# Performance work log

Hardware: AMD Instinct MI355X
Metric: run time of the kernel (lower is better)

## Reference

```python
import jax, jax.numpy as jnp
import numpy as np


def _conv1d(x, w, b):
    # x: (N, C_in, L), w: (C_out, C_in, K=5), padding=2, stride=1 (torch Conv1d semantics)
    y = jax.lax.conv_general_dilated(x, w, window_strides=(1,), padding=[(2, 2)],
                                     dimension_numbers=('NCH', 'OIH', 'NCH'))
    return y + b[None, :, None]


def _conv_block(x, w, b):
    # Conv1d -> ReLU -> MaxPool1d(kernel=2, stride=2)
    y = jax.nn.relu(_conv1d(x, w, b))
    n, c, l = y.shape
    return y.reshape(n, c, l // 2, 2).max(axis=-1)


def setup_inputs() -> dict:
    key = jax.random.key(0)
    ks = jax.random.split(key, 20)

    def lin(k, shape, fan_in):
        bound = 1.0 / np.sqrt(fan_in)
        return jax.random.uniform(k, shape, jnp.float32, -bound, bound)

    inp = {
        'x': jax.random.normal(ks[0], (1, 64, 1024), jnp.float32),
        'topo_map': jax.random.uniform(ks[1], (64, 64), jnp.float32),
        # 64 stacked tiny attention nets: Linear(64->128), Linear(128->64), no bias
        'W1': lin(ks[2], (64, 128, 64), 64),
        'W2': lin(ks[3], (64, 64, 128), 128),
        'c1_w': lin(ks[4], (32, 64, 5), 64 * 5),  'c1_b': lin(ks[5], (32,), 64 * 5),
        'c2_w': lin(ks[6], (16, 32, 5), 32 * 5),  'c2_b': lin(ks[7], (16,), 32 * 5),
        'c3_w': lin(ks[8], (8, 16, 5), 16 * 5),   'c3_b': lin(ks[9], (8,), 16 * 5),
        'c4_w': lin(ks[10], (4, 8, 5), 8 * 5),    'c4_b': lin(ks[11], (4,), 8 * 5),
        'c5_w': lin(ks[12], (2, 4, 5), 4 * 5),    'c5_b': lin(ks[13], (2,), 4 * 5),
        'c6_w': lin(ks[14], (1, 2, 5), 2 * 5),    'c6_b': lin(ks[15], (1,), 2 * 5),
        'out_w': lin(ks[16], (1, 16), 16),        'out_b': lin(ks[17], (1,), 16),
    }
    return inp


def reference(x, topo_map, W1, W2, c1_w, c1_b, c2_w, c2_b, c3_w, c3_b,
              c4_w, c4_b, c5_w, c5_b, c6_w, c6_b, out_w, out_b):
    # xmean: (1, 64) -- mean over time of the single trial
    xmean = x[0].mean(axis=1)[None, :]
    att = xmean * topo_map                                  # (64, 64); row i fed to net i
    # Batched replacement for the 64 sequential tiny MLPs (no CPU round-trip):
    h = jax.nn.relu(jnp.einsum('ik,ihk->ih', att, W1))      # (64, 128)
    attn = jax.nn.sigmoid(jnp.einsum('ih,ioh->io', h, W2))  # (64, 64)
    y = attn[None] @ x                                      # (1, 64, 1024)
    for w, b in ((c1_w, c1_b), (c2_w, c2_b), (c3_w, c3_b),
                 (c4_w, c4_b), (c5_w, c5_b), (c6_w, c6_b)):
        y = _conv_block(y, w, b)                            # L halves each block: 1024 -> 16
    out = y @ out_w.T + out_b                               # (1, 1, 16) @ (16, 1) -> (1, 1, 1)
    return out.reshape(1, 1)
```

## Files before the change

kernel.cpp:

```cpp
#include <hip/hip_runtime.h>
#include <math.h>

__global__ __launch_bounds__(256) void k_xmean(const float* __restrict__ x,
                                               double* __restrict__ xmean) {
    const int c = blockIdx.x;
    const int t = threadIdx.x;
    const float* row = x + c * 1024;
    double s = 0.0;
#pragma unroll
    for (int u = 0; u < 4; ++u) s += (double)row[t + u * 256];
#pragma unroll
    for (int off = 32; off >= 1; off >>= 1) s += __shfl_down(s, off, 64);
    __shared__ double wsum[4];
    if ((t & 63) == 0) wsum[t >> 6] = s;
    __syncthreads();
    if (t == 0) xmean[c] = (wsum[0] + wsum[1] + wsum[2] + wsum[3]) * (1.0 / 1024.0);
}

__global__ __launch_bounds__(256) void k_mlp(const float* __restrict__ topo,
                                             const float* __restrict__ W1,
                                             const float* __restrict__ W2,
                                             const double* __restrict__ xmean,
                                             double* __restrict__ attn) {
    const int i = blockIdx.x;
    const int t = threadIdx.x;
    __shared__ double att[64];
    __shared__ double h[128];
    if (t < 64) att[t] = xmean[t] * (double)topo[i * 64 + t];
    __syncthreads();
    {
        const int hh = t >> 1, half = t & 1;
        const float4* wp = (const float4*)(W1 + i * 8192 + hh * 64 + half * 32);
        double acc = 0.0;
#pragma unroll
        for (int q = 0; q < 8; ++q) {
            float4 w = wp[q];
            const int k = half * 32 + q * 4;
            acc += att[k + 0] * (double)w.x + att[k + 1] * (double)w.y +
                   att[k + 2] * (double)w.z + att[k + 3] * (double)w.w;
        }
        acc += __shfl_xor(acc, 1, 64);
        if (half == 0) h[hh] = acc > 0.0 ? acc : 0.0;
    }
    __syncthreads();
    {
        const int o = t >> 2, part = t & 3;
        const float4* wp = (const float4*)(W2 + i * 8192 + o * 128 + part * 32);
        double acc = 0.0;
#pragma unroll
        for (int q = 0; q < 8; ++q) {
            float4 w = wp[q];
            const int k = part * 32 + q * 4;
            acc += h[k + 0] * (double)w.x + h[k + 1] * (double)w.y +
                   h[k + 2] * (double)w.z + h[k + 3] * (double)w.w;
        }
        acc += __shfl_xor(acc, 1, 64);
        acc += __shfl_xor(acc, 2, 64);
        if (part == 0) attn[i * 64 + o] = 1.0 / (1.0 + exp(-acc));
    }
}

__global__ __launch_bounds__(256) void k_front(const float* __restrict__ x,
                                               const double* __restrict__ attn_g,
                                               const float* __restrict__ c1w,
                                               const float* __restrict__ c1b,
                                               const float* __restrict__ c2w,
                                               const float* __restrict__ c2b,
                                               float* __restrict__ s2out) {
    const int b = blockIdx.x;
    const int t = threadIdx.x;
    const int p0 = b * 2;
    const int lbase = 8 * b - 6;
    const int rbase = 4 * b - 2;

    __shared__ float attn_l[64 * 64];
    __shared__ float x_l[64 * 20];
    __shared__ float y_l[64 * 20];
    __shared__ float w2_l[16 * 32 * 5];
    __shared__ float b1_l[32];
    __shared__ float b2_l[16];
    __shared__ float c1_l[32 * 8];
    __shared__ float c2pre[16 * 4];

    for (int e = t; e < 4096; e += 256) attn_l[e] = (float)attn_g[e];
    for (int e = t; e < 64 * 20; e += 256) {
        const int j = e / 20, li = e % 20, l = lbase + li;
        x_l[e] = (l >= 0 && l < 1024) ? x[j * 1024 + l] : 0.f;
    }
    for (int e = t; e < 2560; e += 256) w2_l[e] = c2w[e];
    if (t < 32) b1_l[t] = c1b[t];
    if (t < 16) b2_l[t] = c2b[t];
    __syncthreads();

    if (t < 128) {
        const int ig = t >> 2, lg = t & 3;
        const int i0 = ig * 2, l0 = lg * 5;
        double acc0[5] = {0, 0, 0, 0, 0}, acc1[5] = {0, 0, 0, 0, 0};
        for (int j = 0; j < 64; ++j) {
            const double a0 = (double)attn_l[i0 * 64 + j];
            const double a1 = (double)attn_l[(i0 + 1) * 64 + j];
#pragma unroll
            for (int c = 0; c < 5; ++c) {
                const double xv = (double)x_l[j * 20 + l0 + c];
                acc0[c] += a0 * xv;
                acc1[c] += a1 * xv;
            }
        }
#pragma unroll
        for (int c = 0; c < 5; ++c) {
            y_l[i0 * 20 + l0 + c]       = (float)acc0[c];
            y_l[(i0 + 1) * 20 + l0 + c] = (float)acc1[c];
        }
    }
    __syncthreads();

    {
        const int oc = t >> 3, rg = (t >> 2) & 1, icq = t & 3;
        const int sb = 8 * rg;
        double acc[8] = {0, 0, 0, 0, 0, 0, 0, 0};
        for (int ic = icq * 16; ic < icq * 16 + 16; ++ic) {
            const float* wrow = &c1w[(oc * 64 + ic) * 5];
            const float* yrow = &y_l[ic * 20 + sb];
            float yv[12];
#pragma unroll
            for (int c = 0; c < 12; ++c) yv[c] = yrow[c];
            float wv[5];
#pragma unroll
            for (int k = 0; k < 5; ++k) wv[k] = wrow[k];
#pragma unroll
            for (int k = 0; k < 5; ++k) {
                const double w = (double)wv[k];
#pragma unroll
                for (int u = 0; u < 8; ++u) acc[u] += w * (double)yv[u + k];
            }
        }
#pragma unroll
        for (int u = 0; u < 8; ++u) {
            acc[u] += __shfl_xor(acc[u], 1, 64);
            acc[u] += __shfl_xor(acc[u], 2, 64);
        }
        if (icq == 0) {
            const double bias = (double)b1_l[oc];
#pragma unroll
            for (int v = 0; v < 4; ++v) {
                const double v0 = acc[2 * v] + bias, v1 = acc[2 * v + 1] + bias;
                const double m = fmax(fmax(v0, v1), 0.0);
                const int r_idx = rg * 4 + v;
                const int r = rbase + r_idx;
                c1_l[oc * 8 + r_idx] = (r >= 0 && r < 512) ? (float)m : 0.f;
            }
        }
    }
    __syncthreads();

    if (t < 64) {
        const int oc = t >> 2, q_idx = t & 3;
        double acc = (double)b2_l[oc];
        for (int ic = 0; ic < 32; ++ic) {
            const float* wrow = &w2_l[(oc * 32 + ic) * 5];
            const float* crow = &c1_l[ic * 8 + q_idx];
#pragma unroll
            for (int k = 0; k < 5; ++k) acc += (double)wrow[k] * (double)crow[k];
        }
        c2pre[t] = (float)fmax(acc, 0.0);
    }
    __syncthreads();
    if (t < 32) {
        const int oc = t >> 1, p_idx = t & 1;
        const float m = fmaxf(c2pre[oc * 4 + 2 * p_idx], c2pre[oc * 4 + 2 * p_idx + 1]);
        s2out[oc * 256 + p0 + p_idx] = m;
    }
}

__global__ __launch_bounds__(256) void k_tail(const float* __restrict__ s2,
                                              const float* __restrict__ c3w, const float* __restrict__ c3b,
                                              const float* __restrict__ c4w, const float* __restrict__ c4b,
                                              const float* __restrict__ c5w, const float* __restrict__ c5b,
                                              const float* __restrict__ c6w, const float* __restrict__ c6b,
                                              const float* __restrict__ ow,  const float* __restrict__ ob,
                                              float* __restrict__ out) {
    const int t = threadIdx.x;
    __shared__ __align__(16) float s2p[16 * 264];
    __shared__ float w3_l[640], b3_l[8];
    __shared__ float s3_l[8 * 128];
    __shared__ float w4_l[160], b4_l[4];
    __shared__ float s4_l[4 * 64];
    __shared__ float w5_l[40],  b5_l[2];
    __shared__ float s5_l[2 * 32];
    __shared__ float w6_l[10],  b6_l[1];
    __shared__ float s6_l[16];
    __shared__ float ow_l[16],  ob_l[1];

    for (int e = t; e < 16 * 264; e += 256) s2p[e] = 0.f;
    for (int e = t; e < 640; e += 256) w3_l[e] = c3w[e];
    if (t < 8)   b3_l[t] = c3b[t];
    if (t < 160) w4_l[t] = c4w[t];
    if (t < 4)   b4_l[t] = c4b[t];
    if (t < 40)  w5_l[t] = c5w[t];
    if (t < 2)   b5_l[t] = c5b[t];
    if (t < 10)  w6_l[t] = c6w[t];
    if (t == 0)  b6_l[0] = c6b[0];
    if (t < 16)  ow_l[t] = ow[t];
    if (t == 0)  ob_l[0] = ob[0];
    __syncthreads();
    for (int e = t; e < 4096; e += 256) {
        const int ic = e >> 8, col = e & 255;
        s2p[ic * 264 + 4 + col] = s2[e];
    }
    __syncthreads();

    {
        const int oc = t >> 5, pg = t & 31;
        double acc[8] = {0, 0, 0, 0, 0, 0, 0, 0};
        for (int ic = 0; ic < 16; ++ic) {
            const float4* win4 = (const float4*)&s2p[ic * 264 + 8 * pg];
            float win[16];
#pragma unroll
            for (int q = 0; q < 4; ++q) {
                const float4 v = win4[q];
                win[4 * q] = v.x; win[4 * q + 1] = v.y; win[4 * q + 2] = v.z; win[4 * q + 3] = v.w;
            }
            const float* wrow = &w3_l[(oc * 16 + ic) * 5];
#pragma unroll
            for (int k = 0; k < 5; ++k) {
                const double w = (double)wrow[k];
#pragma unroll
                for (int u = 0; u < 8; ++u) acc[u] += w * (double)win[u + k + 2];
            }
        }
        const double bias = (double)b3_l[oc];
#pragma unroll
        for (int v = 0; v < 4; ++v) {
            const double v0 = acc[2 * v] + bias, v1 = acc[2 * v + 1] + bias;
            s3_l[oc * 128 + pg * 4 + v] = (float)fmax(fmax(v0, v1), 0.0);
        }
    }
    __syncthreads();

    {
        const int oc = t >> 6, p = t & 63;
        double a0 = (double)b4_l[oc], a1 = a0;
        for (int ic = 0; ic < 8; ++ic) {
            const float* wrow = &w4_l[(oc * 8 + ic) * 5];
            const float* srow = &s3_l[ic * 128];
            float c[6];
#pragma unroll
            for (int u = 0; u < 6; ++u) {
                const int col = 2 * p - 2 + u;
                c[u] = (col >= 0 && col < 128) ? srow[col] : 0.f;
            }
#pragma unroll
            for (int k = 0; k < 5; ++k) {
                const double w = (double)wrow[k];
                a0 += w * (double)c[k];
                a1 += w * (double)c[k + 1];
            }
        }
        s4_l[oc * 64 + p] = (float)fmax(fmax(a0, a1), 0.0);
    }
    __syncthreads();

    if (t < 64) {
        const int oc = t >> 5, p = t & 31;
        double a0 = (double)b5_l[oc], a1 = a0;
        for (int ic = 0; ic < 4; ++ic) {
            const float* wrow = &w5_l[(oc * 4 + ic) * 5];
            const float* srow = &s4_l[ic * 64];
            float c[6];
#pragma unroll
            for (int u = 0; u < 6; ++u) {
                const int col = 2 * p - 2 + u;
                c[u] = (col >= 0 && col < 64) ? srow[col] : 0.f;
            }
#pragma unroll
            for (int k = 0; k < 5; ++k) {
                const double w = (double)wrow[k];
                a0 += w * (double)c[k];
                a1 += w * (double)c[k + 1];
            }
        }
        s5_l[oc * 32 + p] = (float)fmax(fmax(a0, a1), 0.0);
    }
    __syncthreads();

    if (t < 16) {
        const int p = t;
        double a0 = (double)b6_l[0], a1 = a0;
        for (int ic = 0; ic < 2; ++ic) {
            const float* wrow = &w6_l[ic * 5];
            const float* srow = &s5_l[ic * 32];
            float c[6];
#pragma unroll
            for (int u = 0; u < 6; ++u) {
                const int col = 2 * p - 2 + u;
                c[u] = (col >= 0 && col < 32) ? srow[col] : 0.f;
            }
#pragma unroll
            for (int k = 0; k < 5; ++k) {
                const double w = (double)wrow[k];
                a0 += w * (double)c[k];
                a1 += w * (double)c[k + 1];
            }
        }
        s6_l[p] = (float)fmax(fmax(a0, a1), 0.0);
    }
    __syncthreads();

    if (t == 0) {
        double acc = (double)ob_l[0];
#pragma unroll
        for (int l = 0; l < 16; ++l) acc += (double)ow_l[l] * (double)s6_l[l];
        out[0] = (float)acc;
    }
}

extern "C" void kernel_launch(void* const* d_in, const int* in_sizes, int n_in,
                              void* d_out, int out_size, void* d_ws, size_t ws_size,
                              hipStream_t stream) {
    (void)in_sizes; (void)n_in; (void)out_size; (void)ws_size;
    const float* x    = (const float*)d_in[0];
    const float* topo = (const float*)d_in[1];
    const float* W1   = (const float*)d_in[2];
    const float* W2   = (const float*)d_in[3];
    const float* c1w  = (const float*)d_in[4];
    const float* c1b  = (const float*)d_in[5];
    const float* c2w  = (const float*)d_in[6];
    const float* c2b  = (const float*)d_in[7];
    const float* c3w  = (const float*)d_in[8];
    const float* c3b  = (const float*)d_in[9];
    const float* c4w  = (const float*)d_in[10];
    const float* c4b  = (const float*)d_in[11];
    const float* c5w  = (const float*)d_in[12];
    const float* c5b  = (const float*)d_in[13];
    const float* c6w  = (const float*)d_in[14];
    const float* c6b  = (const float*)d_in[15];
    const float* ow   = (const float*)d_in[16];
    const float* ob   = (const float*)d_in[17];

    double* ws_xmean = (double*)d_ws;
    double* ws_attn  = ws_xmean + 64;
    float*  ws_s2    = (float*)(ws_attn + 4096);

    k_xmean<<<64, 256, 0, stream>>>(x, ws_xmean);
    k_mlp<<<64, 256, 0, stream>>>(topo, W1, W2, ws_xmean, ws_attn);
    k_front<<<128, 256, 0, stream>>>(x, ws_attn, c1w, c1b, c2w, c2b, ws_s2);
    k_tail<<<1, 256, 0, stream>>>(ws_s2, c3w, c3b, c4w, c4b, c5w, c5b,
                                  c6w, c6b, ow, ob, (float*)d_out);
}
```

Measured before the change: 124.6 us.

## Fuse all stages into one cooperative kernel with grid-wide syncs

Merges the four kernels (xmean, MLP, front convs, tail convs) into a single cooperative launch of 128 blocks, with grid.sync() between phases instead of separate kernel launches. Each of the 64 MLP blocks now recomputes the full channel mean itself rather than reading it from a separate reduction kernel, and attn is stored as float instead of double to halve that traffic. This removes three launch gaps but adds redundant mean work, grid-barrier cost, and a large combined shared-memory footprint per block.

After: 190.7 us. +53.1%, slower.

```diff
diff --git a/kernel.cpp b/kernel.cpp
--- a/kernel.cpp
+++ b/kernel.cpp
@@ -1,78 +1,29 @@
 #include <hip/hip_runtime.h>
+#include <hip/hip_cooperative_groups.h>
 #include <math.h>
 
-__global__ __launch_bounds__(256) void k_xmean(const float* __restrict__ x,
-                                               double* __restrict__ xmean) {
-    const int c = blockIdx.x;
+namespace cg = cooperative_groups;
+
+__global__ __launch_bounds__(256) void k_fused(
+    const float* __restrict__ x,   const float* __restrict__ topo,
+    const float* __restrict__ W1,  const float* __restrict__ W2,
+    const float* __restrict__ c1w, const float* __restrict__ c1b,
+    const float* __restrict__ c2w, const float* __restrict__ c2b,
+    const float* __restrict__ c3w, const float* __restrict__ c3b,
+    const float* __restrict__ c4w, const float* __restrict__ c4b,
+    const float* __restrict__ c5w, const float* __restrict__ c5b,
+    const float* __restrict__ c6w, const float* __restrict__ c6b,
+    const float* __restrict__ ow,  const float* __restrict__ ob,
+    float* __restrict__ attn_g, float* __restrict__ s2_g,
+    float* __restrict__ out)
+{
+    cg::grid_group grid = cg::this_grid();
     const int t = threadIdx.x;
-    const float* row = x + c * 1024;
-    double s = 0.0;
-#pragma unroll
-    for (int u = 0; u < 4; ++u) s += (double)row[t + u * 256];
-#pragma unroll
-    for (int off = 32; off >= 1; off >>= 1) s += __shfl_down(s, off, 64);
-    __shared__ double wsum[4];
-    if ((t & 63) == 0) wsum[t >> 6] = s;
-    __syncthreads();
-    if (t == 0) xmean[c] = (wsum[0] + wsum[1] + wsum[2] + wsum[3]) * (1.0 / 1024.0);
-}
-
-__global__ __launch_bounds__(256) void k_mlp(const float* __restrict__ topo,
-                                             const float* __restrict__ W1,
-                                             const float* __restrict__ W2,
-                                             const double* __restrict__ xmean,
-                                             double* __restrict__ attn) {
-    const int i = blockIdx.x;
-    const int t = threadIdx.x;
+    const int b = blockIdx.x;
+
+    __shared__ double xm[64];
     __shared__ double att[64];
     __shared__ double h[128];
-    if (t < 64) att[t] = xmean[t] * (double)topo[i * 64 + t];
-    __syncthreads();
-    {
-        const int hh = t >> 1, half = t & 1;
-        const float4* wp = (const float4*)(W1 + i * 8192 + hh * 64 + half * 32);
-        double acc = 0.0;
-#pragma unroll
-        for (int q = 0; q < 8; ++q) {
-            float4 w = wp[q];
-            const int k = half * 32 + q * 4;
-            acc += att[k + 0] * (double)w.x + att[k + 1] * (double)w.y +
-                   att[k + 2] * (double)w.z + att[k + 3] * (double)w.w;
-        }
-        acc += __shfl_xor(acc, 1, 64);
-        if (half == 0) h[hh] = acc > 0.0 ? acc : 0.0;
-    }
-    __syncthreads();
-    {
-        const int o = t >> 2, part = t & 3;
-        const float4* wp = (const float4*)(W2 + i * 8192 + o * 128 + part * 32);
-        double acc = 0.0;
-#pragma unroll
-        for (int q = 0; q < 8; ++q) {
-            float4 w = wp[q];
-            const int k = part * 32 + q * 4;
-            acc += h[k + 0] * (double)w.x + h[k + 1] * (double)w.y +
-                   h[k + 2] * (double)w.z + h[k + 3] * (double)w.w;
-        }
-        acc += __shfl_xor(acc, 1, 64);
-        acc += __shfl_xor(acc, 2, 64);
-        if (part == 0) attn[i * 64 + o] = 1.0 / (1.0 + exp(-acc));
-    }
-}
-
-__global__ __launch_bounds__(256) void k_front(const float* __restrict__ x,
-                                               const double* __restrict__ attn_g,
-                                               const float* __restrict__ c1w,
-                                               const float* __restrict__ c1b,
-                                               const float* __restrict__ c2w,
-                                               const float* __restrict__ c2b,
-                                               float* __restrict__ s2out) {
-    const int b = blockIdx.x;
-    const int t = threadIdx.x;
-    const int p0 = b * 2;
-    const int lbase = 8 * b - 6;
-    const int rbase = 4 * b - 2;
-
     __shared__ float attn_l[64 * 64];
     __shared__ float x_l[64 * 20];
     __shared__ float y_l[64 * 20];
@@ -81,105 +32,6 @@
     __shared__ float b2_l[16];
     __shared__ float c1_l[32 * 8];
     __shared__ float c2pre[16 * 4];
-
-    for (int e = t; e < 4096; e += 256) attn_l[e] = (float)attn_g[e];
-    for (int e = t; e < 64 * 20; e += 256) {
-        const int j = e / 20, li = e % 20, l = lbase + li;
-        x_l[e] = (l >= 0 && l < 1024) ? x[j * 1024 + l] : 0.f;
-    }
-    for (int e = t; e < 2560; e += 256) w2_l[e] = c2w[e];
-    if (t < 32) b1_l[t] = c1b[t];
-    if (t < 16) b2_l[t] = c2b[t];
-    __syncthreads();
-
-    if (t < 128) {
-        const int ig = t >> 2, lg = t & 3;
-        const int i0 = ig * 2, l0 = lg * 5;
-        double acc0[5] = {0, 0, 0, 0, 0}, acc1[5] = {0, 0, 0, 0, 0};
-        for (int j = 0; j < 64; ++j) {
-            const double a0 = (double)attn_l[i0 * 64 + j];
-            const double a1 = (double)attn_l[(i0 + 1) * 64 + j];
-#pragma unroll
-            for (int c = 0; c < 5; ++c) {
-                const double xv = (double)x_l[j * 20 + l0 + c];
-                acc0[c] += a0 * xv;
-                acc1[c] += a1 * xv;
-            }
-        }
-#pragma unroll
-        for (int c = 0; c < 5; ++c) {
-            y_l[i0 * 20 + l0 + c]       = (float)acc0[c];
-            y_l[(i0 + 1) * 20 + l0 + c] = (float)acc1[c];
-        }
-    }
-    __syncthreads();
-
-    {
-        const int oc = t >> 3, rg = (t >> 2) & 1, icq = t & 3;
-        const int sb = 8 * rg;
-        double acc[8] = {0, 0, 0, 0, 0, 0, 0, 0};
-        for (int ic = icq * 16; ic < icq * 16 + 16; ++ic) {
-            const float* wrow = &c1w[(oc * 64 + ic) * 5];
-            const float* yrow = &y_l[ic * 20 + sb];
-            float yv[12];
-#pragma unroll
-            for (int c = 0; c < 12; ++c) yv[c] = yrow[c];
-            float wv[5];
-#pragma unroll
-            for (int k = 0; k < 5; ++k) wv[k] = wrow[k];
-#pragma unroll
-            for (int k = 0; k < 5; ++k) {
-                const double w = (double)wv[k];
-#pragma unroll
-                for (int u = 0; u < 8; ++u) acc[u] += w * (double)yv[u + k];
-            }
-        }
-#pragma unroll
-        for (int u = 0; u < 8; ++u) {
-            acc[u] += __shfl_xor(acc[u], 1, 64);
-            acc[u] += __shfl_xor(acc[u], 2, 64);
-        }
-        if (icq == 0) {
-            const double bias = (double)b1_l[oc];
-#pragma unroll
-            for (int v = 0; v < 4; ++v) {
-                const double v0 = acc[2 * v] + bias, v1 = acc[2 * v + 1] + bias;
-                const double m = fmax(fmax(v0, v1), 0.0);
-                const int r_idx = rg * 4 + v;
-                const int r = rbase + r_idx;
-                c1_l[oc * 8 + r_idx] = (r >= 0 && r < 512) ? (float)m : 0.f;
-            }
-        }
-    }
-    __syncthreads();
-
-    if (t < 64) {
-        const int oc = t >> 2, q_idx = t & 3;
-        double acc = (double)b2_l[oc];
-        for (int ic = 0; ic < 32; ++ic) {
-            const float* wrow = &w2_l[(oc * 32 + ic) * 5];
-            const float* crow = &c1_l[ic * 8 + q_idx];
-#pragma unroll
-            for (int k = 0; k < 5; ++k) acc += (double)wrow[k] * (double)crow[k];
-        }
-        c2pre[t] = (float)fmax(acc, 0.0);
-    }
-    __syncthreads();
-    if (t < 32) {
-        const int oc = t >> 1, p_idx = t & 1;
-        const float m = fmaxf(c2pre[oc * 4 + 2 * p_idx], c2pre[oc * 4 + 2 * p_idx + 1]);
-        s2out[oc * 256 + p0 + p_idx] = m;
-    }
-}
-
-__global__ __launch_bounds__(256) void k_tail(const float* __restrict__ s2,
-                                              const float* __restrict__ c3w, const float* __restrict__ c3b,
-                                              const float* __restrict__ c4w, const float* __restrict__ c4b,
-                                              const float* __restrict__ c5w, const float* __restrict__ c5b,
-                                              const float* __restrict__ c6w, const float* __restrict__ c6b,
-                                              const float* __restrict__ ow,  const float* __restrict__ ob,
-                                              float* __restrict__ out) {
-    const int t = threadIdx.x;
     __shared__ __align__(16) float s2p[16 * 264];
     __shared__ float w3_l[640], b3_l[8];
     __shared__ float s3_l[8 * 128];
@@ -191,126 +43,281 @@
     __shared__ float s6_l[16];
     __shared__ float ow_l[16],  ob_l[1];
 
-    for (int e = t; e < 16 * 264; e += 256) s2p[e] = 0.f;
-    for (int e = t; e < 640; e += 256) w3_l[e] = c3w[e];
-    if (t < 8)   b3_l[t] = c3b[t];
-    if (t < 160) w4_l[t] = c4w[t];
-    if (t < 4)   b4_l[t] = c4b[t];
-    if (t < 40)  w5_l[t] = c5w[t];
-    if (t < 2)   b5_l[t] = c5b[t];
-    if (t < 10)  w6_l[t] = c6w[t];
-    if (t == 0)  b6_l[0] = c6b[0];
-    if (t < 16)  ow_l[t] = ow[t];
-    if (t == 0)  ob_l[0] = ob[0];
-    __syncthreads();
-    for (int e = t; e < 4096; e += 256) {
-        const int ic = e >> 8, col = e & 255;
-        s2p[ic * 264 + 4 + col] = s2[e];
+    if (b < 64) {
+        {
+            const int c = t >> 2, q = t & 3;
+            const float4* xr = (const float4*)(x + c * 1024 + q * 256);
+            double s = 0.0;
+#pragma unroll
+            for (int u = 0; u < 64; ++u) {
+                const float4 v = xr[u];
+                s += (double)v.x + (double)v.y + (double)v.z + (double)v.w;
+            }
+            s += __shfl_xor(s, 1, 64);
+            s += __shfl_xor(s, 2, 64);
+            if (q == 0) xm[c] = s * (1.0 / 1024.0);
+        }
+        __syncthreads();
+        if (t < 64) att[t] = xm[t] * (double)topo[b * 64 + t];
+        __syncthreads();
+        {
+            const int hh = t >> 1, half = t & 1;
+            const float4* wp = (const float4*)(W1 + b * 8192 + hh * 64 + half * 32);
+            double acc = 0.0;
+#pragma unroll
+            for (int q = 0; q < 8; ++q) {
+                const float4 w = wp[q];
+                const int k = half * 32 + q * 4;
+                acc += att[k + 0] * (double)w.x + att[k + 1] * (double)w.y +
+                       att[k + 2] * (double)w.z + att[k + 3] * (double)w.w;
+            }
+            acc += __shfl_xor(acc, 1, 64);
+            if (half == 0) h[hh] = acc > 0.0 ? acc : 0.0;
+        }
+        __syncthreads();
+        {
+            const int o = t >> 2, part = t & 3;
+            const float4* wp = (const float4*)(W2 + b * 8192 + o * 128 + part * 32);
+            double acc = 0.0;
+#pragma unroll
+            for (int q = 0; q < 8; ++q) {
+                const float4 w = wp[q];
+                const int k = part * 32 + q * 4;
+                acc += h[k + 0] * (double)w.x + h[k + 1] * (double)w.y +
+                       h[k + 2] * (double)w.z + h[k + 3] * (double)w.w;
+            }
+            acc += __shfl_xor(acc, 1, 64);
+            acc += __shfl_xor(acc, 2, 64);
+            if (part == 0) attn_g[b * 64 + o] = (float)(1.0 / (1.0 + exp(-acc)));
+        }
     }
-    __syncthreads();
+
+    grid.sync();
 
     {
-        const int oc = t >> 5, pg = t & 31;
-        double acc[8] = {0, 0, 0, 0, 0, 0, 0, 0};
-        for (int ic = 0; ic < 16; ++ic) {
-            const float4* win4 = (const float4*)&s2p[ic * 264 + 8 * pg];
-            float win[16];
-#pragma unroll
-            for (int q = 0; q < 4; ++q) {
-                const float4 v = win4[q];
-                win[4 * q] = v.x; win[4 * q + 1] = v.y; win[4 * q + 2] = v.z; win[4 * q + 3] = v.w;
-            }
-            const float* wrow = &w3_l[(oc * 16 + ic) * 5];
-#pragma unroll
-            for (int k = 0; k < 5; ++k) {
-                const double w = (double)wrow[k];
-#pragma unroll
-                for (int u = 0; u < 8; ++u) acc[u] += w * (double)win[u + k + 2];
-            }
-        }
-        const double bias = (double)b3_l[oc];
-#pragma unroll
-        for (int v = 0; v < 4; ++v) {
-            const double v0 = acc[2 * v] + bias, v1 = acc[2 * v + 1] + bias;
-            s3_l[oc * 128 + pg * 4 + v] = (float)fmax(fmax(v0, v1), 0.0);
+        const int p0 = b * 2;
+        const int lbase = 8 * b - 6;
+        const int rbase = 4 * b - 2;
+
+        {
+            const float4* ag = (const float4*)attn_g;
+            float4* al = (float4*)attn_l;
+            for (int e = t; e < 1024; e += 256) al[e] = ag[e];
+        }
+        for (int e = t; e < 64 * 20; e += 256) {
+            const int j = e / 20, li = e % 20, l = lbase + li;
+            x_l[e] = (l >= 0 && l < 1024) ? x[j * 1024 + l] : 0.f;
+        }
+        for (int e = t; e < 2560; e += 256) w2_l[e] = c2w[e];
+        if (t < 32) b1_l[t] = c1b[t];
+        if (t < 16) b2_l[t] = c2b[t];
+        __syncthreads();
+
+        if (t < 128) {
+            const int ig = t >> 2, lg = t & 3;
+            const int i0 = ig * 2, l0 = lg * 5;
+            double acc0[5] = {0, 0, 0, 0, 0}, acc1[5] = {0, 0, 0, 0, 0};
+            for (int j = 0; j < 64; ++j) {
+                const double a0 = (double)attn_l[i0 * 64 + j];
+                const double a1 = (double)attn_l[(i0 + 1) * 64 + j];
+#pragma unroll
+                for (int c = 0; c < 5; ++c) {
+                    const double xv = (double)x_l[j * 20 + l0 + c];
+                    acc0[c] += a0 * xv;
+                    acc1[c] += a1 * xv;
+                }
+            }
+#pragma unroll
+            for (int c = 0; c < 5; ++c) {
+                y_l[i0 * 20 + l0 + c]       = (float)acc0[c];
+                y_l[(i0 + 1) * 20 + l0 + c] = (float)acc1[c];
+            }
+        }
+        __syncthreads();
+
+        {
+            const int oc = t >> 3, rg = (t >> 2) & 1, icq = t & 3;
+            const int sb = 8 * rg;
+            double acc[8] = {0, 0, 0, 0, 0, 0, 0, 0};
+            for (int ic = icq * 16; ic < icq * 16 + 16; ++ic) {
+                const float* wrow = &c1w[(oc * 64 + ic) * 5];
+                const float* yrow = &y_l[ic * 20 + sb];
+                float yv[12];
+#pragma unroll
+                for (int c = 0; c < 12; ++c) yv[c] = yrow[c];
+                float wv[5];
+#pragma unroll
+                for (int k = 0; k < 5; ++k) wv[k] = wrow[k];
+#pragma unroll
+                for (int k = 0; k < 5; ++k) {
+                    const double w = (double)wv[k];
+#pragma unroll
+                    for (int u = 0; u < 8; ++u) acc[u] += w * (double)yv[u + k];
+                }
+            }
+#pragma unroll
+            for (int u = 0; u < 8; ++u) {
+                acc[u] += __shfl_xor(acc[u], 1, 64);
+                acc[u] += __shfl_xor(acc[u], 2, 64);
+            }
+            if (icq == 0) {
+                const double bias = (double)b1_l[oc];
+#pragma unroll
+                for (int v = 0; v < 4; ++v) {
+                    const double v0 = acc[2 * v] + bias, v1 = acc[2 * v + 1] + bias;
+                    const double m = fmax(fmax(v0, v1), 0.0);
+                    const int r_idx = rg * 4 + v;
+                    const int r = rbase + r_idx;
+                    c1_l[oc * 8 + r_idx] = (r >= 0 && r < 512) ? (float)m : 0.f;
+                }
+            }
+        }
+        __syncthreads();
+
+        if (t < 64) {
+            const int oc = t >> 2, q_idx = t & 3;
+            double acc = (double)b2_l[oc];
+            for (int ic = 0; ic < 32; ++ic) {
+                const float* wrow = &w2_l[(oc * 32 + ic) * 5];
+                const float* crow = &c1_l[ic * 8 + q_idx];
+#pragma unroll
+                for (int k = 0; k < 5; ++k) acc += (double)wrow[k] * (double)crow[k];
+            }
+            c2pre[t] = (float)fmax(acc, 0.0);
+        }
+        __syncthreads();
+        if (t < 32) {
+            const int oc = t >> 1, p_idx = t & 1;
+            const float m = fmaxf(c2pre[oc * 4 + 2 * p_idx], c2pre[oc * 4 + 2 * p_idx + 1]);
+            s2_g[oc * 256 + p0 + p_idx] = m;
         }
     }
-    __syncthreads();
-
-    {
-        const int oc = t >> 6, p = t & 63;
-        double a0 = (double)b4_l[oc], a1 = a0;
-        for (int ic = 0; ic < 8; ++ic) {
-            const float* wrow = &w4_l[(oc * 8 + ic) * 5];
-            const float* srow = &s3_l[ic * 128];
-            float c[6];
-#pragma unroll
-            for (int u = 0; u < 6; ++u) {
-                const int col = 2 * p - 2 + u;
-                c[u] = (col >= 0 && col < 128) ? srow[col] : 0.f;
-            }
-#pragma unroll
-            for (int k = 0; k < 5; ++k) {
-                const double w = (double)wrow[k];
-                a0 += w * (double)c[k];
-                a1 += w * (double)c[k + 1];
-            }
-        }
-        s4_l[oc * 64 + p] = (float)fmax(fmax(a0, a1), 0.0);
-    }
-    __syncthreads();
-
-    if (t < 64) {
-        const int oc = t >> 5, p = t & 31;
-        double a0 = (double)b5_l[oc], a1 = a0;
-        for (int ic = 0; ic < 4; ++ic) {
-            const float* wrow = &w5_l[(oc * 4 + ic) * 5];
-            const float* srow = &s4_l[ic * 64];
-            float c[6];
-#pragma unroll
-            for (int u = 0; u < 6; ++u) {
-                const int col = 2 * p - 2 + u;
-                c[u] = (col >= 0 && col < 64) ? srow[col] : 0.f;
-            }
-#pragma unroll
-            for (int k = 0; k < 5; ++k) {
-                const double w = (double)wrow[k];
-                a0 += w * (double)c[k];
-                a1 += w * (double)c[k + 1];
-            }
-        }
-        s5_l[oc * 32 + p] = (float)fmax(fmax(a0, a1), 0.0);
-    }
-    __syncthreads();
-
-    if (t < 16) {
-        const int p = t;
-        double a0 = (double)b6_l[0], a1 = a0;
-        for (int ic = 0; ic < 2; ++ic) {
-            const float* wrow = &w6_l[ic * 5];
-            const float* srow = &s5_l[ic * 32];
-            float c[6];
-#pragma unroll
-            for (int u = 0; u < 6; ++u) {
-                const int col = 2 * p - 2 + u;
-                c[u] = (col >= 0 && col < 32) ? srow[col] : 0.f;
-            }
-#pragma unroll
-            for (int k = 0; k < 5; ++k) {
-                const double w = (double)wrow[k];
-                a0 += w * (double)c[k];
-                a1 += w * (double)c[k + 1];
-            }
-        }
-        s6_l[p] = (float)fmax(fmax(a0, a1), 0.0);
-    }
-    __syncthreads();
-
-    if (t == 0) {
-        double acc = (double)ob_l[0];
-#pragma unroll
-        for (int l = 0; l < 16; ++l) acc += (double)ow_l[l] * (double)s6_l[l];
-        out[0] = (float)acc;
+
+    grid.sync();
+
+    if (b == 0) {
+        for (int e = t; e < 16 * 264; e += 256) s2p[e] = 0.f;
+        for (int e = t; e < 640; e += 256) w3_l[e] = c3w[e];
+        if (t < 8)   b3_l[t] = c3b[t];
+        if (t < 160) w4_l[t] = c4w[t];
+        if (t < 4)   b4_l[t] = c4b[t];
+        if (t < 40)  w5_l[t] = c5w[t];
+        if (t < 2)   b5_l[t] = c5b[t];
+        if (t < 10)  w6_l[t] = c6w[t];
+        if (t == 0)  b6_l[0] = c6b[0];
+        if (t < 16)  ow_l[t] = ow[t];
+        if (t == 0)  ob_l[0] = ob[0];
+        __syncthreads();
+        for (int e = t; e < 4096; e += 256) {
+            const int ic = e >> 8, col = e & 255;
+            s2p[ic * 264 + 4 + col] = s2_g[e];
+        }
+        __syncthreads();
+
+        {
+            const int oc = t >> 5, pg = t & 31;
+            double acc[8] = {0, 0, 0, 0, 0, 0, 0, 0};
+            for (int ic = 0; ic < 16; ++ic) {
+                const float4* win4 = (const float4*)&s2p[ic * 264 + 8 * pg];
+                float win[16];
+#pragma unroll
+                for (int q = 0; q < 4; ++q) {
+                    const float4 v = win4[q];
+                    win[4 * q] = v.x; win[4 * q + 1] = v.y;
+                    win[4 * q + 2] = v.z; win[4 * q + 3] = v.w;
+                }
+                const float* wrow = &w3_l[(oc * 16 + ic) * 5];
+#pragma unroll
+                for (int k = 0; k < 5; ++k) {
+                    const double w = (double)wrow[k];
+#pragma unroll
+                    for (int u = 0; u < 8; ++u) acc[u] += w * (double)win[u + k + 2];
+                }
+            }
+            const double bias = (double)b3_l[oc];
+#pragma unroll
+            for (int v = 0; v < 4; ++v) {
+                const double v0 = acc[2 * v] + bias, v1 = acc[2 * v + 1] + bias;
+                s3_l[oc * 128 + pg * 4 + v] = (float)fmax(fmax(v0, v1), 0.0);
+            }
+        }
+        __syncthreads();
+
+        {
+            const int oc = t >> 6, p = t & 63;
+            double a0 = (double)b4_l[oc], a1 = a0;
+            for (int ic = 0; ic < 8; ++ic) {
+                const float* wrow = &w4_l[(oc * 8 + ic) * 5];
+                const float* srow = &s3_l[ic * 128];
+                float c[6];
+#pragma unroll
+                for (int u = 0; u < 6; ++u) {
+                    const int col = 2 * p - 2 + u;
+                    c[u] = (col >= 0 && col < 128) ? srow[col] : 0.f;
+                }
+#pragma unroll
+                for (int k = 0; k < 5; ++k) {
+                    const double w = (double)wrow[k];
+                    a0 += w * (double)c[k];
+                    a1 += w * (double)c[k + 1];
+                }
+            }
+            s4_l[oc * 64 + p] = (float)fmax(fmax(a0, a1), 0.0);
+        }
+        __syncthreads();
+
+        if (t < 64) {
+            const int oc = t >> 5, p = t & 31;
+            double a0 = (double)b5_l[oc], a1 = a0;
+            for (int ic = 0; ic < 4; ++ic) {
+                const float* wrow = &w5_l[(oc * 4 + ic) * 5];
+                const float* srow = &s4_l[ic * 64];
+                float c[6];
+#pragma unroll
+                for (int u = 0; u < 6; ++u) {
+                    const int col = 2 * p - 2 + u;
+                    c[u] = (col >= 0 && col < 64) ? srow[col] : 0.f;
+                }
+#pragma unroll
+                for (int k = 0; k < 5; ++k) {
+                    const double w = (double)wrow[k];
+                    a0 += w * (double)c[k];
+                    a1 += w * (double)c[k + 1];
+                }
+            }
+            s5_l[oc * 32 + p] = (float)fmax(fmax(a0, a1), 0.0);
+        }
+        __syncthreads();
+
+        if (t < 16) {
+            const int p = t;
+            double a0 = (double)b6_l[0], a1 = a0;
+            for (int ic = 0; ic < 2; ++ic) {
+                const float* wrow = &w6_l[ic * 5];
+                const float* srow = &s5_l[ic * 32];
+                float c[6];
+#pragma unroll
+                for (int u = 0; u < 6; ++u) {
+                    const int col = 2 * p - 2 + u;
+                    c[u] = (col >= 0 && col < 32) ? srow[col] : 0.f;
+                }
+#pragma unroll
+                for (int k = 0; k < 5; ++k) {
+                    const double w = (double)wrow[k];
+                    a0 += w * (double)c[k];
+                    a1 += w * (double)c[k + 1];
+                }
+            }
+            s6_l[p] = (float)fmax(fmax(a0, a1), 0.0);
+        }
+        __syncthreads();
+
+        if (t == 0) {
+            double acc = (double)ob_l[0];
+#pragma unroll
+            for (int l = 0; l < 16; ++l) acc += (double)ow_l[l] * (double)s6_l[l];
+            out[0] = (float)acc;
+        }
     }
 }
 
@@ -337,13 +344,17 @@
     const float* ow   = (const float*)d_in[16];
     const float* ob   = (const float*)d_in[17];
 
-    double* ws_xmean = (double*)d_ws;
-    double* ws_attn  = ws_xmean + 64;
-    float*  ws_s2    = (float*)(ws_attn + 4096);
-
-    k_xmean<<<64, 256, 0, stream>>>(x, ws_xmean);
-    k_mlp<<<64, 256, 0, stream>>>(topo, W1, W2, ws_xmean, ws_attn);
-    k_front<<<128, 256, 0, stream>>>(x, ws_attn, c1w, c1b, c2w, c2b, ws_s2);
-    k_tail<<<1, 256, 0, stream>>>(ws_s2, c3w, c3b, c4w, c4b, c5w, c5b,
-                                  c6w, c6b, ow, ob, (float*)d_out);
+    float* ws_attn = (float*)d_ws;
+    float* ws_s2   = ws_attn + 4096;
+    float* outf    = (float*)d_out;
+
+    void* args[] = {
+        (void*)&x,   (void*)&topo, (void*)&W1,  (void*)&W2,
+        (void*)&c1w, (void*)&c1b,  (void*)&c2w, (void*)&c2b,
+        (void*)&c3w, (void*)&c3b,  (void*)&c4w, (void*)&c4b,
+        (void*)&c5w, (void*)&c5b,  (void*)&c6w, (void*)&c6b,
+        (void*)&ow,  (void*)&ob,
+        (void*)&ws_attn, (void*)&ws_s2, (void*)&outf,
+    };
+    hipLaunchCooperativeKernel((void*)k_fused, dim3(128), dim3(256), args, 0, stream);
 }
```
